# Kernel tuning notes

Measured on AMD Instinct MI355X. Metric: run time of the kernel, lower is better.

The kernel has to match this reference:

```python
import jax, jax.numpy as jnp
import numpy as np

C = 512
C8 = C // 8  # 64
B, H, W = 4, 64, 64


def setup_inputs() -> dict:
    key = jax.random.key(0)
    ks = jax.random.split(key, 8)
    s_in = 1.0 / np.sqrt(C)
    return {
        "x": jax.random.normal(ks[0], (B, C, H, W), dtype=jnp.float32),
        "Wf": jax.random.normal(ks[1], (C8, C), dtype=jnp.float32) * s_in,
        "bf": jax.random.normal(ks[2], (C8,), dtype=jnp.float32) * 0.01,
        "Wg": jax.random.normal(ks[3], (C8, C), dtype=jnp.float32) * s_in,
        "bg": jax.random.normal(ks[4], (C8,), dtype=jnp.float32) * 0.01,
        "Wh": jax.random.normal(ks[5], (C, C), dtype=jnp.float32) * s_in,
        "bh": jax.random.normal(ks[6], (C,), dtype=jnp.float32) * 0.01,
        # original inits gamma=0; use small nonzero so the attention path is exercised
        "gamma": jax.random.normal(ks[7], (1,), dtype=jnp.float32) * 0.1,
    }


def reference(x, Wf, bf, Wg, bg, Wh, bh, gamma):
    b, c, h, w = x.shape
    n = h * w
    xt = x.reshape(b, c, n)  # flatten spatial -> tokens (b, C, N)
    # 1x1 convs are per-token GEMMs
    f = jnp.einsum('bcn,oc->bno', xt, Wf) + bf          # (b, N, C8)
    g = jnp.einsum('bcn,oc->bon', xt, Wg) + bg[:, None]  # (b, C8, N)
    attn = jax.nn.softmax(jnp.einsum('bnk,bkm->bnm', f, g), axis=2)  # (b, N, N)
    hv = jnp.einsum('bcn,oc->bon', xt, Wh) + bh[:, None]  # (b, C, N)
    # torch.bmm(h, attention): out[:,c,j] = sum_i h[:,c,i] * attn[:,i,j]
    sa = jnp.einsum('bci,bij->bcj', hv, attn).reshape(b, c, h, w)
    return gamma[0] * sa + x
```

## Files before the change

### kernel.cpp

```cpp
#include <hip/hip_runtime.h>


#define Bq 4
#define Cq 512
#define Nq 4096
#define PSTR 88

typedef __attribute__((ext_vector_type(8))) short bf16x8;
typedef __attribute__((ext_vector_type(4))) float f32x4;

__device__ __forceinline__ short f2bf(float f) {
  unsigned u = __float_as_uint(f);
  u += 0x7fffu + ((u >> 16) & 1u);
  return (short)(u >> 16);
}
__device__ __forceinline__ float bf2f(short h) {
  return __uint_as_float(((unsigned)(unsigned short)h) << 16);
}

#define MFMA16(A, B, C) __builtin_amdgcn_mfma_f32_16x16x32_bf16((A), (B), (C), 0, 0, 0)

__device__ __forceinline__ size_t fg_frag(int b, int t16, int ss) {
  return ((size_t)((b * 256 + t16) * 2 + ss)) * 512;
}
__device__ __forceinline__ size_t hv_frag(int b, int tc, int si) {
  return ((size_t)((b * 32 + tc) * 128 + si)) * 512;
}

__global__ __launch_bounds__(256) void k_prepw(
    const float* __restrict__ Wf, const float* __restrict__ Wg,
    const float* __restrict__ Wh,
    short* __restrict__ whi, short* __restrict__ wlo, short* __restrict__ whb) {
  int gid = blockIdx.x * 256 + threadIdx.x;
  if (gid < 128 * 512) {
    int row = gid >> 9;
    float v = (row < 64) ? Wf[gid] : Wg[gid - 32768];
    short h = f2bf(v);
    whi[gid] = h;
    wlo[gid] = f2bf(v - bf2f(h));
  }
  whb[gid] = f2bf(Wh[gid]);
}

__global__ __launch_bounds__(256) void k_xpose(
    const float* __restrict__ x, short* __restrict__ xthi, short* __restrict__ xtlo) {
  int b = blockIdx.z, c0 = blockIdx.y * 64, n0 = blockIdx.x * 64;
  __shared__ float tile[64][65];
  int t = threadIdx.x;
  int l = t & 15, g = t >> 4;
  const float* xp = x + ((size_t)b * Cq + c0) * Nq + n0;
#pragma unroll
  for (int e = 0; e < 4; e++) {
    int cl = g + e * 16;
    float4 v = *(const float4*)(xp + (size_t)cl * Nq + l * 4);
    tile[cl][l * 4 + 0] = v.x; tile[cl][l * 4 + 1] = v.y;
    tile[cl][l * 4 + 2] = v.z; tile[cl][l * 4 + 3] = v.w;
  }
  __syncthreads();
#pragma unroll
  for (int e = 0; e < 4; e++) {
    int nl = g + e * 16;
    short hi[4], lo[4];
#pragma unroll
    for (int qq = 0; qq < 4; qq++) {
      float v = tile[l * 4 + qq][nl];
      hi[qq] = f2bf(v);
      lo[qq] = f2bf(v - bf2f(hi[qq]));
    }
    size_t off = ((size_t)b * Nq + n0 + nl) * Cq + c0 + l * 4;
    *(short4*)(xthi + off) = make_short4(hi[0], hi[1], hi[2], hi[3]);
    *(short4*)(xtlo + off) = make_short4(lo[0], lo[1], lo[2], lo[3]);
  }
}

__global__ __launch_bounds__(512) void k_fg(
    const short* __restrict__ xthi, const short* __restrict__ xtlo,
    const short* __restrict__ whi, const short* __restrict__ wlo,
    const float* __restrict__ bfv, const float* __restrict__ bgv,
    short* __restrict__ ffh, short* __restrict__ ffl,
    short* __restrict__ gfh, short* __restrict__ gfl) {
  int b = blockIdx.y, n0 = blockIdx.x * 64;
  int t = threadIdx.x, w = t >> 6, lane = t & 63, l15 = lane & 15, q = lane >> 4;
  int wr = w & 3, wh = w >> 2;
  const short* ah = xthi + ((size_t)b * Nq + n0 + wr * 16 + l15) * Cq;
  const short* al = xtlo + ((size_t)b * Nq + n0 + wr * 16 + l15) * Cq;
  f32x4 z = {0.f, 0.f, 0.f, 0.f};
  f32x4 acc[4] = {z, z, z, z};
  for (int ks = 0; ks < 16; ks++) {
    bf16x8 Ahi = *(const bf16x8*)(ah + ks * 32 + q * 8);
    bf16x8 Alo = *(const bf16x8*)(al + ks * 32 + q * 8);
#pragma unroll
    for (int os = 0; os < 4; os++) {
      int o = wh * 64 + os * 16 + l15;
      bf16x8 Bhi = *(const bf16x8*)(whi + o * 512 + ks * 32 + q * 8);
      bf16x8 Blo = *(const bf16x8*)(wlo + o * 512 + ks * 32 + q * 8);
      acc[os] = MFMA16(Alo, Bhi, acc[os]);
      acc[os] = MFMA16(Ahi, Blo, acc[os]);
      acc[os] = MFMA16(Ahi, Bhi, acc[os]);
    }
  }
#pragma unroll
  for (int os = 0; os < 4; os++) {
#pragma unroll
    for (int r = 0; r < 4; r++) {
      int o = os * 16 + l15;
      int n = n0 + wr * 16 + q * 4 + r;
      float v = acc[os][r] + (wh == 0 ? bfv[o] : bgv[o]);
      size_t off = ((size_t)((b * 256 + (n >> 4)) * 2 + (o >> 5))) * 512
                 + (((o >> 3) & 3) * 16 + (n & 15)) * 8 + (o & 7);
      short h = f2bf(v);
      short lo = f2bf(v - bf2f(h));
      if (wh == 0) { ffh[off] = h; ffl[off] = lo; }
      else         { gfh[off] = h; gfl[off] = lo; }
    }
  }
}

__global__ __launch_bounds__(512) void k_stats(
    const short* __restrict__ ffh, const short* __restrict__ ffl,
    const short* __restrict__ gfh, const short* __restrict__ gfl,
    float* __restrict__ lsum) {
  int jc = blockIdx.x * 1024, i0 = blockIdx.y * 64, b = blockIdx.z;
  int t = threadIdx.x, w = t >> 6, lane = t & 63, l15 = lane & 15, q = lane >> 4;
  bf16x8 Ahi[4][2], Alo[4][2];
#pragma unroll
  for (int ig = 0; ig < 4; ig++)
#pragma unroll
    for (int ss = 0; ss < 2; ss++) {
      size_t base = fg_frag(b, (i0 >> 4) + ig, ss) + lane * 8;
      Ahi[ig][ss] = *(const bf16x8*)(ffh + base);
      Alo[ig][ss] = *(const bf16x8*)(ffl + base);
    }
  float ls[16];
#pragma unroll
  for (int a = 0; a < 16; a++) ls[a] = 0.f;
  f32x4 z = {0.f, 0.f, 0.f, 0.f};
  for (int jt = 0; jt < 8; jt++) {
    int tj = (jc >> 4) + w * 8 + jt;
    bf16x8 GBh[2], GBl[2];
#pragma unroll
    for (int ss = 0; ss < 2; ss++) {
      size_t base = fg_frag(b, tj, ss) + lane * 8;
      GBh[ss] = *(const bf16x8*)(gfh + base);
      GBl[ss] = *(const bf16x8*)(gfl + base);
    }
#pragma unroll
    for (int ig = 0; ig < 4; ig++) {
      f32x4 sh = z, sl = z;
#pragma unroll
      for (int ss = 0; ss < 2; ss++) {
        sl = MFMA16(Alo[ig][ss], GBh[ss], sl);
        sl = MFMA16(Ahi[ig][ss], GBl[ss], sl);
        sh = MFMA16(Ahi[ig][ss], GBh[ss], sh);
      }
#pragma unroll
      for (int r = 0; r < 4; r++) ls[ig * 4 + r] += __expf(sh[r] + sl[r]);
    }
  }
#pragma unroll
  for (int m = 1; m < 16; m <<= 1) {
#pragma unroll
    for (int a = 0; a < 16; a++) ls[a] += __shfl_xor(ls[a], m, 64);
  }
  __shared__ float part[8][64];
  if (l15 == 0) {
#pragma unroll
    for (int ig = 0; ig < 4; ig++)
#pragma unroll
      for (int r = 0; r < 4; r++) part[w][ig * 16 + q * 4 + r] = ls[ig * 4 + r];
  }
  __syncthreads();
  if (t < 64) {
    float s = 0.f;
#pragma unroll
    for (int ww = 0; ww < 8; ww++) s += part[ww][t];
    atomicAdd(&lsum[(size_t)b * Nq + i0 + t], s);
  }
}

__global__ __launch_bounds__(512) void k_hv(
    const short* __restrict__ whb, const short* __restrict__ xthi,
    const float* __restrict__ bhv, const float* __restrict__ lsum,
    short* __restrict__ hvf) {
  int si = blockIdx.x, b = blockIdx.y;
  int t = threadIdx.x, w = t >> 6, lane = t & 63, l15 = lane & 15, q = lane >> 4;
  int c0 = w * 64;
  const short* ar0 = xthi + ((size_t)b * Nq + si * 32 + l15) * Cq;
  const short* ar1 = ar0 + 16 * Cq;
  f32x4 z = {0.f, 0.f, 0.f, 0.f};
  f32x4 acc[2][4];
#pragma unroll
  for (int a = 0; a < 2; a++)
#pragma unroll
    for (int c = 0; c < 4; c++) acc[a][c] = z;
  for (int ks = 0; ks < 16; ks++) {
    bf16x8 A0 = *(const bf16x8*)(ar0 + ks * 32 + q * 8);
    bf16x8 A1 = *(const bf16x8*)(ar1 + ks * 32 + q * 8);
#pragma unroll
    for (int ct = 0; ct < 4; ct++) {
      bf16x8 Bv = *(const bf16x8*)(whb + (size_t)(c0 + ct * 16 + l15) * 512 + ks * 32 + q * 8);
      acc[0][ct] = MFMA16(A0, Bv, acc[0][ct]);
      acc[1][ct] = MFMA16(A1, Bv, acc[1][ct]);
    }
  }
  float li[2][4];
#pragma unroll
  for (int it = 0; it < 2; it++)
#pragma unroll
    for (int r = 0; r < 4; r++)
      li[it][r] = 1.0f / lsum[(size_t)b * Nq + si * 32 + it * 16 + q * 4 + r];
  int src0 = ((q & 1) << 5) + l15;
  int src1 = src0 + 16;
  int hiSel = q >> 1;
#pragma unroll
  for (int ct = 0; ct < 4; ct++) {
    float bias = bhv[c0 + ct * 16 + l15];
    unsigned u01[2], u23[2];
#pragma unroll
    for (int it = 0; it < 2; it++) {
      float v0 = (acc[it][ct][0] + bias) * li[it][0];
      float v1 = (acc[it][ct][1] + bias) * li[it][1];
      float v2 = (acc[it][ct][2] + bias) * li[it][2];
      float v3 = (acc[it][ct][3] + bias) * li[it][3];
      u01[it] = (unsigned)(unsigned short)f2bf(v0) | ((unsigned)(unsigned short)f2bf(v1) << 16);
      u23[it] = (unsigned)(unsigned short)f2bf(v2) | ((unsigned)(unsigned short)f2bf(v3) << 16);
    }
    unsigned a0 = __shfl((int)u01[0], src0), b0 = __shfl((int)u01[1], src0);
    unsigned a1 = __shfl((int)u23[0], src0), b1 = __shfl((int)u23[1], src0);
    unsigned a2 = __shfl((int)u01[0], src1), b2 = __shfl((int)u01[1], src1);
    unsigned a3 = __shfl((int)u23[0], src1), b3 = __shfl((int)u23[1], src1);
    uint4 st;
    st.x = hiSel ? b0 : a0;
    st.y = hiSel ? b1 : a1;
    st.z = hiSel ? b2 : a2;
    st.w = hiSel ? b3 : a3;
    *(uint4*)(hvf + hv_frag(b, (c0 >> 4) + ct, si) + (size_t)lane * 8) = st;
  }
}

__global__ __launch_bounds__(512, 2) void k_attn(
    const short* __restrict__ ffh, const short* __restrict__ ffl,
    const short* __restrict__ gfh, const short* __restrict__ gfl,
    const short* __restrict__ hvf, const float* __restrict__ x,
    const float* __restrict__ gp, float* __restrict__ out) {
  int L = blockIdx.x;
  int b = (L & 7) >> 1;
  int ch = L & 1;
  int jt32 = L >> 3;
  int j0 = jt32 * 128, c0 = ch * 256;
  int t = threadIdx.x, w = t >> 6, lane = t & 63, l15 = lane & 15, q = lane >> 4;
  int cg = w & 3, jg = w >> 2;
  __shared__ __align__(16) short pt[2][128 * PSTR];
  float gamma = gp[0];
  f32x4 z = {0.f, 0.f, 0.f, 0.f};
  f32x4 acc[4][4];
#pragma unroll
  for (int a = 0; a < 4; a++)
#pragma unroll
    for (int bb = 0; bb < 4; bb++) acc[a][bb] = z;
  bf16x8 GBh[4][2], GBl[4][2];
#pragma unroll
  for (int jt = 0; jt < 4; jt++)
#pragma unroll
    for (int ss = 0; ss < 2; ss++) {
      size_t base = fg_frag(b, (j0 >> 4) + jg * 4 + jt, ss) + lane * 8;
      GBh[jt][ss] = *(const bf16x8*)(gfh + base);
      GBl[jt][ss] = *(const bf16x8*)(gfl + base);
    }

  auto computeS = [&](int it, int buf) {
    bf16x8 Ah[2], Al[2];
#pragma unroll
    for (int ss = 0; ss < 2; ss++) {
      size_t base = fg_frag(b, it * 4 + cg, ss) + lane * 8;
      Ah[ss] = *(const bf16x8*)(ffh + base);
      Al[ss] = *(const bf16x8*)(ffl + base);
    }
#pragma unroll
    for (int jt = 0; jt < 4; jt++) {
      f32x4 sh = z, sl = z;
#pragma unroll
      for (int ss = 0; ss < 2; ss++) {
        sl = MFMA16(Al[ss], GBh[jt][ss], sl);
        sl = MFMA16(Ah[ss], GBl[jt][ss], sl);
        sh = MFMA16(Ah[ss], GBh[jt][ss], sh);
      }
      unsigned p01 = (unsigned)(unsigned short)f2bf(__expf(sh[0] + sl[0])) |
                     ((unsigned)(unsigned short)f2bf(__expf(sh[1] + sl[1])) << 16);
      unsigned p23 = (unsigned)(unsigned short)f2bf(__expf(sh[2] + sl[2])) |
                     ((unsigned)(unsigned short)f2bf(__expf(sh[3] + sl[3])) << 16);
      uint2 pv; pv.x = p01; pv.y = p23;
      *(uint2*)(&pt[buf][(jg * 64 + jt * 16 + l15) * PSTR + cg * 16 + q * 4]) = pv;
    }
  };

  computeS(0, 0);
  for (int it = 0; it < 64; it++) {
    __syncthreads();
    int buf = it & 1;
    if (it < 63) computeS(it + 1, 1 - buf);
#pragma unroll
    for (int ss = 0; ss < 2; ss++) {
      bf16x8 PB[4];
#pragma unroll
      for (int jt = 0; jt < 4; jt++)
        PB[jt] = *(const bf16x8*)(&pt[buf][(jg * 64 + jt * 16 + l15) * PSTR + ss * 32 + q * 8]);
#pragma unroll
      for (int ct = 0; ct < 4; ct++) {
        size_t hb = hv_frag(b, (c0 >> 4) + cg * 4 + ct, it * 2 + ss) + lane * 8;
        bf16x8 A = *(const bf16x8*)(hvf + hb);
#pragma unroll
        for (int jt = 0; jt < 4; jt++)
          acc[ct][jt] = MFMA16(A, PB[jt], acc[ct][jt]);
      }
    }
  }
#pragma unroll
  for (int ct = 0; ct < 4; ct++) {
#pragma unroll
    for (int jt = 0; jt < 4; jt++) {
#pragma unroll
      for (int r = 0; r < 4; r++) {
        int c = c0 + cg * 64 + ct * 16 + q * 4 + r;
        int j = j0 + jg * 64 + jt * 16 + l15;
        size_t off = ((size_t)b * Cq + c) * Nq + j;
        out[off] = gamma * acc[ct][jt][r] + x[off];
      }
    }
  }
}

extern "C" void kernel_launch(void* const* d_in, const int* in_sizes, int n_in,
                              void* d_out, int out_size, void* d_ws, size_t ws_size,
                              hipStream_t stream) {
  (void)in_sizes; (void)n_in; (void)out_size; (void)ws_size;
  const float* x  = (const float*)d_in[0];
  const float* Wf = (const float*)d_in[1];
  const float* bf = (const float*)d_in[2];
  const float* Wg = (const float*)d_in[3];
  const float* bg = (const float*)d_in[4];
  const float* Wh = (const float*)d_in[5];
  const float* bh = (const float*)d_in[6];
  const float* gm = (const float*)d_in[7];
  float* out = (float*)d_out;
  char* ws = (char*)d_ws;
  short* xthi = (short*)(ws);
  short* xtlo = (short*)(ws + 16777216);
  short* ffh  = (short*)(ws + 33554432);
  short* ffl  = (short*)(ws + 35651584);
  short* gfh  = (short*)(ws + 37748736);
  short* gfl  = (short*)(ws + 39845888);
  short* whi  = (short*)(ws + 41943040);
  short* wlo  = (short*)(ws + 42074112);
  short* whb  = (short*)(ws + 42205184);
  float* lsum = (float*)(ws + 42729472);
  short* hvf  = (short*)(ws + 42795008);

  hipLaunchKernelGGL(k_prepw, dim3(1024), dim3(256), 0, stream, Wf, Wg, Wh, whi, wlo, whb);
  hipLaunchKernelGGL(k_xpose, dim3(64, 8, 4), dim3(256), 0, stream, x, xthi, xtlo);
  hipLaunchKernelGGL(k_fg, dim3(64, 4), dim3(512), 0, stream,
                     xthi, xtlo, whi, wlo, bf, bg, ffh, ffl, gfh, gfl);
  hipMemsetAsync(lsum, 0, 65536, stream);
  hipLaunchKernelGGL(k_stats, dim3(4, 64, 4), dim3(512), 0, stream, ffh, ffl, gfh, gfl, lsum);
  hipLaunchKernelGGL(k_hv, dim3(128, 4), dim3(512), 0, stream, whb, xthi, bh, lsum, hvf);
  hipLaunchKernelGGL(k_attn, dim3(256), dim3(512), 0, stream,
                     ffh, ffl, gfh, gfl, hvf, x, gm, out);
}
```

Baseline: 349.9 us.

## Retile attention kernel to full-channel 64-column tiles and drop atomic row sums

```diff
diff --git a/kernel.cpp b/kernel.cpp
--- a/kernel.cpp
+++ b/kernel.cpp
@@ -4,7 +4,7 @@
 #define Bq 4
 #define Cq 512
 #define Nq 4096
-#define PSTR 88
+#define PSTR 72
 
 typedef __attribute__((ext_vector_type(8))) short bf16x8;
 typedef __attribute__((ext_vector_type(4))) float f32x4;
@@ -119,8 +119,8 @@
 __global__ __launch_bounds__(512) void k_stats(
     const short* __restrict__ ffh, const short* __restrict__ ffl,
     const short* __restrict__ gfh, const short* __restrict__ gfl,
-    float* __restrict__ lsum) {
-  int jc = blockIdx.x * 1024, i0 = blockIdx.y * 64, b = blockIdx.z;
+    float* __restrict__ lsum4) {
+  int jch = blockIdx.x, jc = jch * 1024, i0 = blockIdx.y * 64, b = blockIdx.z;
   int t = threadIdx.x, w = t >> 6, lane = t & 63, l15 = lane & 15, q = lane >> 4;
   bf16x8 Ahi[4][2], Alo[4][2];
 #pragma unroll
@@ -174,13 +174,13 @@
     float s = 0.f;
 #pragma unroll
     for (int ww = 0; ww < 8; ww++) s += part[ww][t];
-    atomicAdd(&lsum[(size_t)b * Nq + i0 + t], s);
+    lsum4[(size_t)jch * 16384 + (size_t)b * Nq + i0 + t] = s;
   }
 }
 
 __global__ __launch_bounds__(512) void k_hv(
     const short* __restrict__ whb, const short* __restrict__ xthi,
-    const float* __restrict__ bhv, const float* __restrict__ lsum,
+    const float* __restrict__ bhv, const float* __restrict__ lsum4,
     short* __restrict__ hvf) {
   int si = blockIdx.x, b = blockIdx.y;
   int t = threadIdx.x, w = t >> 6, lane = t & 63, l15 = lane & 15, q = lane >> 4;
@@ -207,8 +207,11 @@
 #pragma unroll
   for (int it = 0; it < 2; it++)
 #pragma unroll
-    for (int r = 0; r < 4; r++)
-      li[it][r] = 1.0f / lsum[(size_t)b * Nq + si * 32 + it * 16 + q * 4 + r];
+    for (int r = 0; r < 4; r++) {
+      size_t idx = (size_t)b * Nq + si * 32 + it * 16 + q * 4 + r;
+      float s = lsum4[idx] + lsum4[16384 + idx] + lsum4[32768 + idx] + lsum4[49152 + idx];
+      li[it][r] = 1.0f / s;
+    }
   int src0 = ((q & 1) << 5) + l15;
   int src1 = src0 + 16;
   int hiSel = q >> 1;
@@ -245,12 +248,11 @@
     const float* __restrict__ gp, float* __restrict__ out) {
   int L = blockIdx.x;
   int b = (L & 7) >> 1;
-  int ch = L & 1;
-  int jt32 = L >> 3;
-  int j0 = jt32 * 128, c0 = ch * 256;
+  int jt64 = ((L >> 3) << 1) | (L & 1);
+  int j0 = jt64 * 64;
   int t = threadIdx.x, w = t >> 6, lane = t & 63, l15 = lane & 15, q = lane >> 4;
-  int cg = w & 3, jg = w >> 2;
-  __shared__ __align__(16) short pt[2][128 * PSTR];
+  int iq = w & 3, jh = w >> 2;
+  __shared__ __align__(16) short pt[2][64 * PSTR];
   float gamma = gp[0];
   f32x4 z = {0.f, 0.f, 0.f, 0.f};
   f32x4 acc[4][4];
@@ -258,12 +260,12 @@
   for (int a = 0; a < 4; a++)
 #pragma unroll
     for (int bb = 0; bb < 4; bb++) acc[a][bb] = z;
-  bf16x8 GBh[4][2], GBl[4][2];
-#pragma unroll
-  for (int jt = 0; jt < 4; jt++)
-#pragma unroll
-    for (int ss = 0; ss < 2; ss++) {
-      size_t base = fg_frag(b, (j0 >> 4) + jg * 4 + jt, ss) + lane * 8;
+  bf16x8 GBh[2][2], GBl[2][2];
+#pragma unroll
+  for (int jt = 0; jt < 2; jt++)
+#pragma unroll
+    for (int ss = 0; ss < 2; ss++) {
+      size_t base = fg_frag(b, (j0 >> 4) + jh * 2 + jt, ss) + lane * 8;
       GBh[jt][ss] = *(const bf16x8*)(gfh + base);
       GBl[jt][ss] = *(const bf16x8*)(gfl + base);
     }
@@ -272,12 +274,12 @@
     bf16x8 Ah[2], Al[2];
 #pragma unroll
     for (int ss = 0; ss < 2; ss++) {
-      size_t base = fg_frag(b, it * 4 + cg, ss) + lane * 8;
+      size_t base = fg_frag(b, it * 4 + iq, ss) + lane * 8;
       Ah[ss] = *(const bf16x8*)(ffh + base);
       Al[ss] = *(const bf16x8*)(ffl + base);
     }
 #pragma unroll
-    for (int jt = 0; jt < 4; jt++) {
+    for (int jt = 0; jt < 2; jt++) {
       f32x4 sh = z, sl = z;
 #pragma unroll
       for (int ss = 0; ss < 2; ss++) {
@@ -290,7 +292,7 @@
       unsigned p23 = (unsigned)(unsigned short)f2bf(__expf(sh[2] + sl[2])) |
                      ((unsigned)(unsigned short)f2bf(__expf(sh[3] + sl[3])) << 16);
       uint2 pv; pv.x = p01; pv.y = p23;
-      *(uint2*)(&pt[buf][(jg * 64 + jt * 16 + l15) * PSTR + cg * 16 + q * 4]) = pv;
+      *(uint2*)(&pt[buf][(jh * 32 + jt * 16 + l15) * PSTR + iq * 16 + q * 4]) = pv;
     }
   };
 
@@ -304,10 +306,10 @@
       bf16x8 PB[4];
 #pragma unroll
       for (int jt = 0; jt < 4; jt++)
-        PB[jt] = *(const bf16x8*)(&pt[buf][(jg * 64 + jt * 16 + l15) * PSTR + ss * 32 + q * 8]);
+        PB[jt] = *(const bf16x8*)(&pt[buf][(jt * 16 + l15) * PSTR + ss * 32 + q * 8]);
 #pragma unroll
       for (int ct = 0; ct < 4; ct++) {
-        size_t hb = hv_frag(b, (c0 >> 4) + cg * 4 + ct, it * 2 + ss) + lane * 8;
+        size_t hb = hv_frag(b, w * 4 + ct, it * 2 + ss) + lane * 8;
         bf16x8 A = *(const bf16x8*)(hvf + hb);
 #pragma unroll
         for (int jt = 0; jt < 4; jt++)
@@ -321,8 +323,8 @@
     for (int jt = 0; jt < 4; jt++) {
 #pragma unroll
       for (int r = 0; r < 4; r++) {
-        int c = c0 + cg * 64 + ct * 16 + q * 4 + r;
-        int j = j0 + jg * 64 + jt * 16 + l15;
+        int c = w * 64 + ct * 16 + q * 4 + r;
+        int j = j0 + jt * 16 + l15;
         size_t off = ((size_t)b * Cq + c) * Nq + j;
         out[off] = gamma * acc[ct][jt][r] + x[off];
       }
@@ -344,25 +346,24 @@
   const float* gm = (const float*)d_in[7];
   float* out = (float*)d_out;
   char* ws = (char*)d_ws;
-  short* xthi = (short*)(ws);
-  short* xtlo = (short*)(ws + 16777216);
-  short* ffh  = (short*)(ws + 33554432);
-  short* ffl  = (short*)(ws + 35651584);
-  short* gfh  = (short*)(ws + 37748736);
-  short* gfl  = (short*)(ws + 39845888);
-  short* whi  = (short*)(ws + 41943040);
-  short* wlo  = (short*)(ws + 42074112);
-  short* whb  = (short*)(ws + 42205184);
-  float* lsum = (float*)(ws + 42729472);
-  short* hvf  = (short*)(ws + 42795008);
+  short* xthi  = (short*)(ws);
+  short* xtlo  = (short*)(ws + 16777216);
+  short* ffh   = (short*)(ws + 33554432);
+  short* ffl   = (short*)(ws + 35651584);
+  short* gfh   = (short*)(ws + 37748736);
+  short* gfl   = (short*)(ws + 39845888);
+  short* whi   = (short*)(ws + 41943040);
+  short* wlo   = (short*)(ws + 42074112);
+  short* whb   = (short*)(ws + 42205184);
+  float* lsum4 = (float*)(ws + 42729472);
+  short* hvf   = (short*)(ws + 42991616);
 
   hipLaunchKernelGGL(k_prepw, dim3(1024), dim3(256), 0, stream, Wf, Wg, Wh, whi, wlo, whb);
   hipLaunchKernelGGL(k_xpose, dim3(64, 8, 4), dim3(256), 0, stream, x, xthi, xtlo);
   hipLaunchKernelGGL(k_fg, dim3(64, 4), dim3(512), 0, stream,
                      xthi, xtlo, whi, wlo, bf, bg, ffh, ffl, gfh, gfl);
-  hipMemsetAsync(lsum, 0, 65536, stream);
-  hipLaunchKernelGGL(k_stats, dim3(4, 64, 4), dim3(512), 0, stream, ffh, ffl, gfh, gfl, lsum);
-  hipLaunchKernelGGL(k_hv, dim3(128, 4), dim3(512), 0, stream, whb, xthi, bh, lsum, hvf);
+  hipLaunchKernelGGL(k_stats, dim3(4, 64, 4), dim3(512), 0, stream, ffh, ffl, gfh, gfl, lsum4);
+  hipLaunchKernelGGL(k_hv, dim3(128, 4), dim3(512), 0, stream, whb, xthi, bh, lsum4, hvf);
   hipLaunchKernelGGL(k_attn, dim3(256), dim3(512), 0, stream,
                      ffh, ffl, gfh, gfl, hvf, x, gm, out);
 }
```

After: 338.2 us. 3.3% less time.
